# Kernel tuning notes

Measured on AMD Instinct MI355X. Metric: run time of the kernel, lower is better.

## Reference

```python
import jax, jax.numpy as jnp
import numpy as np

H = 2048   # hidden_size
I = 4096   # intermediate_size (expert_dim_per_shard, world_size=1)
E = 8      # num_local_experts


def setup_inputs() -> dict:
    key = jax.random.key(0)
    ks = jax.random.split(key, 7)
    s = 0.02
    return {
        "hidden_states": jax.random.normal(ks[0], (1, 2048, H), dtype=jnp.float32),
        "router_w": jax.random.normal(ks[1], (H, E), dtype=jnp.float32) * s,
        "gate_up_proj": jax.random.normal(ks[2], (E, H, 2 * I), dtype=jnp.float32) * s,
        "down_proj": jax.random.normal(ks[3], (E, I, H), dtype=jnp.float32) * s,
        "shared_gate_w": jax.random.normal(ks[4], (H, I), dtype=jnp.float32) * s,
        "shared_up_w": jax.random.normal(ks[5], (H, I), dtype=jnp.float32) * s,
        "shared_down_w": jax.random.normal(ks[6], (I, H), dtype=jnp.float32) * s,
        "top_k": 1,
    }


def reference(hidden_states, router_w, gate_up_proj, down_proj,
              shared_gate_w, shared_up_w, shared_down_w, top_k):
    b, s, h = hidden_states.shape
    hs = hidden_states.reshape(-1, h)                      # [T, H]
    T = hs.shape[0]

    # router + topk scatter (non-topk -> -inf so sigmoid -> 0)
    logits = hs @ router_w                                 # [T, E]
    top_v, top_i = jax.lax.top_k(logits, top_k)            # [T, k]
    neg_inf = jnp.full_like(logits, -jnp.inf)
    rows = jnp.arange(T)[:, None]
    router_scores = neg_inf.at[rows, top_i].set(top_v).T   # [E, T]
    router_scores = jax.nn.sigmoid(router_scores.astype(jnp.float32)).astype(hs.dtype)

    # dense dispatch: every token to every expert, scaled by (mostly zero) scores
    routed_in = hs[None, :, :] * router_scores[:, :, None]  # [E, T, H]

    # per-expert grouped GEMM (SwiGLU)
    gate_up = jnp.einsum('eth,ehf->etf', routed_in, gate_up_proj)  # [E, T, 2I]
    gate, up = jnp.split(gate_up, 2, axis=-1)
    routed_out = jnp.einsum('eti,eih->eth', up * jax.nn.silu(gate), down_proj)  # [E, T, H]

    # shared expert (SwiGLU MLP)
    shared = (jax.nn.silu(hs @ shared_gate_w) * (hs @ shared_up_w)) @ shared_down_w  # [T, H]

    # scatter_add over arange indices == sum over experts
    out = shared + routed_out.sum(axis=0)                  # [T, H]
    return out, router_scores
```

## Files before the change

### kernel.cpp

```cpp
#include <hip/hip_runtime.h>
#include <hip/hip_bf16.h>

#define H_DIM 2048
#define E_NUM 8
#define I_DIM 4096
#define TWO_I 8192
#define T_TOK 2048

#define BM 256
#define BN 64
#define BK 64

typedef __bf16 bf16x8 __attribute__((ext_vector_type(8)));
typedef float f32x4 __attribute__((ext_vector_type(4)));

static __device__ __forceinline__ unsigned short f2bs(float x) {
    __hip_bfloat16 h = __float2bfloat16(x);
    return __builtin_bit_cast(unsigned short, h);
}

#define GLL(gsrc, ldst) __builtin_amdgcn_global_load_lds( \
    (const __attribute__((address_space(1))) void*)(gsrc), \
    (__attribute__((address_space(3))) void*)(ldst), 16, 0, 0)

#define MFMA16(a, b, c) __builtin_amdgcn_mfma_f32_16x16x32_bf16(a, b, c, 0, 0, 0)
#define BSWZ(n) (((((n) & 7) ^ (((n) >> 2) & 7))) << 4)
#define A_SRC_CHUNK(lane) ((((lane) & 7) ^ (((lane) >> 3) & 7)) * 8)
#define BARRIER() asm volatile("s_waitcnt lgkmcnt(0)\ns_barrier" ::: "memory")

static __device__ __forceinline__ bf16x8 bload(
    const unsigned short* __restrict__ Bs, int n, int s, int h) {
    int off = (n * 128 + s * 64 + h * 16) ^ BSWZ(n);
    return *reinterpret_cast<const bf16x8*>((const char*)Bs + off);
}

static __device__ __forceinline__ bf16x8 aload(
    const unsigned short* __restrict__ As, int row, int s, int h) {
    int off = row * 128 + ((s * 64 + h * 16) ^ ((row & 7) << 4));
    return *reinterpret_cast<const bf16x8*>((const char*)As + off);
}

__global__ __launch_bounds__(256) void router_convert_kernel(
    const float* __restrict__ hs, const float* __restrict__ rw,
    float* __restrict__ out_scores, int* __restrict__ eidx,
    unsigned short* __restrict__ xb, unsigned short* __restrict__ xs) {
    int tok = blockIdx.x * 4 + (threadIdx.x >> 6);
    int lane = threadIdx.x & 63;
    const float* row = hs + (size_t)tok * H_DIM;
    float4 v[8];
    float acc[E_NUM];
#pragma unroll
    for (int e = 0; e < E_NUM; e++) acc[e] = 0.f;
#pragma unroll
    for (int i = 0; i < 8; i++) {
        int hb = i * 256 + lane * 4;
        v[i] = *reinterpret_cast<const float4*>(row + hb);
        const float* w0 = rw + (size_t)hb * E_NUM;
#pragma unroll
        for (int e = 0; e < E_NUM; e++) {
            acc[e] += v[i].x * w0[e] + v[i].y * w0[E_NUM + e] +
                      v[i].z * w0[2 * E_NUM + e] + v[i].w * w0[3 * E_NUM + e];
        }
    }
#pragma unroll
    for (int e = 0; e < E_NUM; e++) {
#pragma unroll
        for (int o = 32; o > 0; o >>= 1) acc[e] += __shfl_xor(acc[e], o, 64);
    }
    int best = 0; float bv = acc[0];
#pragma unroll
    for (int e = 1; e < E_NUM; e++) { if (acc[e] > bv) { bv = acc[e]; best = e; } }
    float sc = 1.f / (1.f + expf(-bv));
    if (lane < E_NUM) out_scores[(size_t)lane * T_TOK + tok] = (lane == best) ? sc : 0.f;
    if (lane == 0) eidx[tok] = best;
    unsigned short* xbr = xb + (size_t)tok * H_DIM;
    unsigned short* xsr = xs + (size_t)tok * H_DIM;
#pragma unroll
    for (int i = 0; i < 8; i++) {
        int hb = i * 256 + lane * 4;
        ushort4 b, s4;
        b.x = f2bs(v[i].x); b.y = f2bs(v[i].y); b.z = f2bs(v[i].z); b.w = f2bs(v[i].w);
        s4.x = f2bs(v[i].x * sc); s4.y = f2bs(v[i].y * sc);
        s4.z = f2bs(v[i].z * sc); s4.w = f2bs(v[i].w * sc);
        *reinterpret_cast<ushort4*>(xbr + hb) = b;
        *reinterpret_cast<ushort4*>(xsr + hb) = s4;
    }
}

__global__ void group_kernel(const int* __restrict__ eidx, int* __restrict__ perm,
                             int* __restrict__ off) {
    __shared__ int cnt[E_NUM];
    __shared__ int base[E_NUM];
    int t = threadIdx.x;
    if (t < E_NUM) cnt[t] = 0;
    __syncthreads();
    for (int i = t; i < T_TOK; i += 256) atomicAdd(&cnt[eidx[i]], 1);
    __syncthreads();
    if (t == 0) {
        int s = 0;
        for (int e = 0; e < E_NUM; e++) { base[e] = s; off[e] = s; s += cnt[e]; }
        off[E_NUM] = s;
    }
    __syncthreads();
    for (int i = t; i < T_TOK; i += 256) {
        int e = eidx[i];
        int p = atomicAdd(&base[e], 1);
        perm[p] = i;
    }
}

__global__ __launch_bounds__(256, 2) void gemm1_kernel(
    const unsigned short* __restrict__ xb, const unsigned short* __restrict__ xs,
    const float* __restrict__ gup, const float* __restrict__ sg,
    const float* __restrict__ su, const int* __restrict__ perm,
    const int* __restrict__ off, unsigned short* __restrict__ hmid) {
    int nt = blockIdx.x;
    int g = blockIdx.y >> 3;
    int mt = blockIdx.y & 7;
    int rowbase, ng;
    if (g < E_NUM) { rowbase = off[g]; ng = off[g + 1] - rowbase; }
    else { rowbase = 0; ng = T_TOK; }
    int mstart = mt * BM;
    if (mstart >= ng) return;

    __shared__ unsigned short As[2][BM * BK];
    __shared__ unsigned short Bg[BN * BK];
    __shared__ unsigned short Bu[BN * BK];

    int tid = threadIdx.x;
    int wave = tid >> 6, lane = tid & 63;
    int h = lane >> 4, ln = lane & 15;

    const unsigned short* Abase = (g == E_NUM) ? xb : xs;
    unsigned int aoff[8];
#pragma unroll
    for (int j = 0; j < 8; j++) {
        int r = wave * 64 + j * 8 + (lane >> 3);
        int sr = mstart + r; sr = (sr < ng) ? sr : (ng - 1);
        int tokr = (g < E_NUM) ? perm[rowbase + sr] : sr;
        aoff[j] = (unsigned int)tokr * H_DIM + A_SRC_CHUNK(lane);
    }
    int n0 = nt * BN;
    const float* gbase;
    const float* ubase;
    size_t ldb;
    if (g < E_NUM) {
        gbase = gup + (size_t)g * H_DIM * TWO_I + n0;
        ubase = gbase + I_DIM;
        ldb = TWO_I;
    } else {
        gbase = sg + n0;
        ubase = su + n0;
        ldb = I_DIM;
    }
    int k0i = wave * 16 + ((lane >> 4) << 2);
    int nb = (lane & 15) << 2;
    const float* pg = gbase + (size_t)k0i * ldb + nb;
    const float* pu = ubase + (size_t)k0i * ldb + nb;

    f32x4 zero = {0.f, 0.f, 0.f, 0.f};
    f32x4 accg[4][4], accu[4][4];
#pragma unroll
    for (int i = 0; i < 4; i++)
#pragma unroll
        for (int j = 0; j < 4; j++) { accg[i][j] = zero; accu[i][j] = zero; }

    const int NT = H_DIM / BK;
    f32x4 qg0, qg1, qg2, qg3, qu0, qu1, qu2, qu3;

#define G1_QLOAD(t_) { size_t ko_ = (size_t)(t_) * BK * ldb; \
        const float* p_ = pg + ko_; \
        qg0 = *reinterpret_cast<const f32x4*>(p_); \
        qg1 = *reinterpret_cast<const f32x4*>(p_ + ldb); \
        qg2 = *reinterpret_cast<const f32x4*>(p_ + 2 * ldb); \
        qg3 = *reinterpret_cast<const f32x4*>(p_ + 3 * ldb); \
        p_ = pu + ko_; \
        qu0 = *reinterpret_cast<const f32x4*>(p_); \
        qu1 = *reinterpret_cast<const f32x4*>(p_ + ldb); \
        qu2 = *reinterpret_cast<const f32x4*>(p_ + 2 * ldb); \
        qu3 = *reinterpret_cast<const f32x4*>(p_ + 3 * ldb); }
#define G1_BWRITE() { _Pragma("unroll") \
        for (int i_ = 0; i_ < 4; i_++) { int n_ = nb + i_; \
            ushort4 og_, ou_; \
            og_.x = f2bs(qg0[i_]); og_.y = f2bs(qg1[i_]); \
            og_.z = f2bs(qg2[i_]); og_.w = f2bs(qg3[i_]); \
            ou_.x = f2bs(qu0[i_]); ou_.y = f2bs(qu1[i_]); \
            ou_.z = f2bs(qu2[i_]); ou_.w = f2bs(qu3[i_]); \
            int ob_ = (n_ * 128 + k0i * 2) ^ BSWZ(n_); \
            *reinterpret_cast<ushort4*>((char*)Bg + ob_) = og_; \
            *reinterpret_cast<ushort4*>((char*)Bu + ob_) = ou_; } }
#define G1_AGLL(t_, buf_) { _Pragma("unroll") \
        for (int j_ = 0; j_ < 8; j_++) \
            GLL(Abase + aoff[j_] + (unsigned)(t_) * BK, \
                &As[buf_][(wave * 64 + j_ * 8) * BK]); }

    G1_QLOAD(0);
    G1_AGLL(0, 0);
    asm volatile("s_waitcnt vmcnt(0)" ::: "memory");
    G1_BWRITE();
    G1_AGLL(1, 1);
    G1_QLOAD(1);
    BARRIER();

    for (int t = 0; t < NT; ++t) {
        const unsigned short* Ab = &As[t & 1][0];
#pragma unroll
        for (int s = 0; s < 2; s++) {
            bf16x8 a0 = aload(Ab, wave * 64 + 0 * 16 + ln, s, h);
            bf16x8 a1 = aload(Ab, wave * 64 + 1 * 16 + ln, s, h);
            bf16x8 a2 = aload(Ab, wave * 64 + 2 * 16 + ln, s, h);
            bf16x8 a3 = aload(Ab, wave * 64 + 3 * 16 + ln, s, h);
#pragma unroll
            for (int j = 0; j < 4; j++) {
                bf16x8 bg = bload(Bg, j * 16 + ln, s, h);
                accg[0][j] = MFMA16(a0, bg, accg[0][j]);
                accg[1][j] = MFMA16(a1, bg, accg[1][j]);
                accg[2][j] = MFMA16(a2, bg, accg[2][j]);
                accg[3][j] = MFMA16(a3, bg, accg[3][j]);
            }
#pragma unroll
            for (int j = 0; j < 4; j++) {
                bf16x8 bu = bload(Bu, j * 16 + ln, s, h);
                accu[0][j] = MFMA16(a0, bu, accu[0][j]);
                accu[1][j] = MFMA16(a1, bu, accu[1][j]);
                accu[2][j] = MFMA16(a2, bu, accu[2][j]);
                accu[3][j] = MFMA16(a3, bu, accu[3][j]);
            }
        }
        BARRIER();
        if (t + 1 < NT) {
            G1_BWRITE();
            int tc = t + 2; if (tc > NT - 1) tc = NT - 1;
            G1_AGLL(tc, t & 1);
            G1_QLOAD(tc);
            BARRIER();
        }
    }

    int hbase = (g < E_NUM) ? rowbase : T_TOK;
#pragma unroll
    for (int i = 0; i < 4; i++) {
#pragma unroll
        for (int j = 0; j < 4; j++) {
#pragma unroll
            for (int r = 0; r < 4; r++) {
                int row = wave * 64 + i * 16 + h * 4 + r;
                int sr = mstart + row;
                if (sr < ng) {
                    float gv = accg[i][j][r], uv = accu[i][j][r];
                    float hv = gv / (1.f + expf(-gv)) * uv;
                    int col = n0 + j * 16 + ln;
                    hmid[(size_t)(hbase + sr) * I_DIM + col] = f2bs(hv);
                }
            }
        }
    }
}

template <int ADD>
__global__ __launch_bounds__(256, 2) void gemm2_kernel(
    const unsigned short* __restrict__ hmid, const float* __restrict__ dwn,
    const float* __restrict__ sd, const int* __restrict__ perm,
    const int* __restrict__ off, float* __restrict__ out) {
    int nt = blockIdx.x;
    int g, mt, rowbase, ng, hbase;
    if (ADD) {
        g = blockIdx.y >> 3; mt = blockIdx.y & 7;
        rowbase = off[g]; ng = off[g + 1] - rowbase; hbase = rowbase;
    } else {
        g = E_NUM; mt = blockIdx.y; rowbase = 0; ng = T_TOK; hbase = T_TOK;
    }
    int mstart = mt * BM;
    if (mstart >= ng) return;

    __shared__ unsigned short As[2][BM * BK];
    __shared__ unsigned short Bs[BN * BK];

    int tid = threadIdx.x;
    int wave = tid >> 6, lane = tid & 63;
    int h = lane >> 4, ln = lane & 15;

    unsigned int aoff[8];
#pragma unroll
    for (int j = 0; j < 8; j++) {
        int r = wave * 64 + j * 8 + (lane >> 3);
        int sr = mstart + r; sr = (sr < ng) ? sr : (ng - 1);
        aoff[j] = (unsigned int)(hbase + sr) * I_DIM + A_SRC_CHUNK(lane);
    }
    int n0 = nt * BN;
    const float* bbase = ADD ? (dwn + (size_t)g * I_DIM * H_DIM + n0) : (sd + n0);
    const size_t ldb = H_DIM;
    int k0i = wave * 16 + ((lane >> 4) << 2);
    int nb = (lane & 15) << 2;
    const float* pb = bbase + (size_t)k0i * ldb + nb;

    f32x4 zero = {0.f, 0.f, 0.f, 0.f};
    f32x4 acc[4][4];
#pragma unroll
    for (int i = 0; i < 4; i++)
#pragma unroll
        for (int j = 0; j < 4; j++) acc[i][j] = zero;

    const int NT2 = I_DIM / BK;
    f32x4 qb0, qb1, qb2, qb3;

#define G2_QLOAD(t_) { size_t ko_ = (size_t)(t_) * BK * ldb; \
        const float* p_ = pb + ko_; \
        qb0 = *reinterpret_cast<const f32x4*>(p_); \
        qb1 = *reinterpret_cast<const f32x4*>(p_ + ldb); \
        qb2 = *reinterpret_cast<const f32x4*>(p_ + 2 * ldb); \
        qb3 = *reinterpret_cast<const f32x4*>(p_ + 3 * ldb); }
#define G2_BWRITE() { _Pragma("unroll") \
        for (int i_ = 0; i_ < 4; i_++) { int n_ = nb + i_; \
            ushort4 o_; \
            o_.x = f2bs(qb0[i_]); o_.y = f2bs(qb1[i_]); \
            o_.z = f2bs(qb2[i_]); o_.w = f2bs(qb3[i_]); \
            int ob_ = (n_ * 128 + k0i * 2) ^ BSWZ(n_); \
            *reinterpret_cast<ushort4*>((char*)Bs + ob_) = o_; } }
#define G2_AGLL(t_, buf_) { _Pragma("unroll") \
        for (int j_ = 0; j_ < 8; j_++) \
            GLL(hmid + aoff[j_] + (unsigned)(t_) * BK, \
                &As[buf_][(wave * 64 + j_ * 8) * BK]); }

    G2_QLOAD(0);
    G2_AGLL(0, 0);
    asm volatile("s_waitcnt vmcnt(0)" ::: "memory");
    G2_BWRITE();
    G2_AGLL(1, 1);
    G2_QLOAD(1);
    BARRIER();

    for (int t = 0; t < NT2; ++t) {
        const unsigned short* Ab = &As[t & 1][0];
#pragma unroll
        for (int s = 0; s < 2; s++) {
            bf16x8 a0 = aload(Ab, wave * 64 + 0 * 16 + ln, s, h);
            bf16x8 a1 = aload(Ab, wave * 64 + 1 * 16 + ln, s, h);
            bf16x8 a2 = aload(Ab, wave * 64 + 2 * 16 + ln, s, h);
            bf16x8 a3 = aload(Ab, wave * 64 + 3 * 16 + ln, s, h);
#pragma unroll
            for (int j = 0; j < 4; j++) {
                bf16x8 b = bload(Bs, j * 16 + ln, s, h);
                acc[0][j] = MFMA16(a0, b, acc[0][j]);
                acc[1][j] = MFMA16(a1, b, acc[1][j]);
                acc[2][j] = MFMA16(a2, b, acc[2][j]);
                acc[3][j] = MFMA16(a3, b, acc[3][j]);
            }
        }
        BARRIER();
        if (t + 1 < NT2) {
            G2_BWRITE();
            int tc = t + 2; if (tc > NT2 - 1) tc = NT2 - 1;
            G2_AGLL(tc, t & 1);
            G2_QLOAD(tc);
            BARRIER();
        }
    }

#pragma unroll
    for (int i = 0; i < 4; i++) {
#pragma unroll
        for (int j = 0; j < 4; j++) {
#pragma unroll
            for (int r = 0; r < 4; r++) {
                int row = wave * 64 + i * 16 + h * 4 + r;
                int sr = mstart + row;
                if (sr < ng) {
                    int tok = ADD ? perm[rowbase + sr] : sr;
                    int col = n0 + j * 16 + ln;
                    float v = acc[i][j][r];
                    float* o = out + (size_t)tok * H_DIM + col;
                    if (ADD) *o += v; else *o = v;
                }
            }
        }
    }
}

extern "C" void kernel_launch(void* const* d_in, const int* in_sizes, int n_in,
                              void* d_out, int out_size, void* d_ws, size_t ws_size,
                              hipStream_t stream) {
    (void)in_sizes; (void)n_in; (void)out_size;
    const float* hs  = (const float*)d_in[0];
    const float* rw  = (const float*)d_in[1];
    const float* gup = (const float*)d_in[2];
    const float* dwn = (const float*)d_in[3];
    const float* sg  = (const float*)d_in[4];
    const float* su  = (const float*)d_in[5];
    const float* sd  = (const float*)d_in[6];
    float* out = (float*)d_out;
    float* out_scores = out + (size_t)T_TOK * H_DIM;

    char* w = (char*)d_ws;
    size_t o = 0;
    auto alloc = [&](size_t bytes) {
        void* p = w + o;
        o += (bytes + 255) & ~(size_t)255;
        return p;
    };
    unsigned short* xb   = (unsigned short*)alloc((size_t)T_TOK * H_DIM * 2);
    unsigned short* xs   = (unsigned short*)alloc((size_t)T_TOK * H_DIM * 2);
    unsigned short* hmid = (unsigned short*)alloc((size_t)2 * T_TOK * I_DIM * 2);
    int* eidx    = (int*)alloc(T_TOK * 4);
    int* perm    = (int*)alloc(T_TOK * 4);
    int* off     = (int*)alloc(64 * 4);
    if (ws_size < o) return;

    router_convert_kernel<<<T_TOK / 4, 256, 0, stream>>>(hs, rw, out_scores, eidx, xb, xs);
    group_kernel<<<1, 256, 0, stream>>>(eidx, perm, off);

    gemm1_kernel<<<dim3(I_DIM / BN, 9 * 8), 256, 0, stream>>>(
        xb, xs, gup, sg, su, perm, off, hmid);
    gemm2_kernel<0><<<dim3(H_DIM / BN, 8), 256, 0, stream>>>(hmid, dwn, sd, perm, off, out);
    gemm2_kernel<1><<<dim3(H_DIM / BN, E_NUM * 8), 256, 0, stream>>>(hmid, dwn, sd, perm, off, out);
}
```

Before: 507.9 us.

## Deepen B-weight register prefetch to two stages with partial vmcnt waits

Both GEMM kernels now keep two register sets of fp32 weight tiles in flight, prefetching the B tile three K-steps ahead instead of two. The main loop is unrolled by two so the register sets alternate, and explicit s_waitcnt vmcnt(N) waits allow only the oldest loads to complete before compute. The aim is to hide global load latency for the fp32 weight stream, which dominates memory traffic. This costs extra VGPRs, which may hurt occupancy at launch bounds of 2 blocks. The hand-counted vmcnt values must match the actual number of outstanding loads.

```diff
diff --git a/kernel.cpp b/kernel.cpp
--- a/kernel.cpp
+++ b/kernel.cpp
@@ -27,6 +27,7 @@
 #define BSWZ(n) (((((n) & 7) ^ (((n) >> 2) & 7))) << 4)
 #define A_SRC_CHUNK(lane) ((((lane) & 7) ^ (((lane) >> 3) & 7)) * 8)
 #define BARRIER() asm volatile("s_waitcnt lgkmcnt(0)\ns_barrier" ::: "memory")
+#define FENCE() asm volatile("" ::: "memory")
 
 static __device__ __forceinline__ bf16x8 bload(
     const unsigned short* __restrict__ Bs, int n, int s, int h) {
@@ -124,8 +125,8 @@
     if (mstart >= ng) return;
 
     __shared__ unsigned short As[2][BM * BK];
-    __shared__ unsigned short Bg[BN * BK];
-    __shared__ unsigned short Bu[BN * BK];
+    __shared__ unsigned short LBg[BN * BK];
+    __shared__ unsigned short LBu[BN * BK];
 
     int tid = threadIdx.x;
     int wave = tid >> 6, lane = tid & 63;
@@ -166,75 +167,85 @@
         for (int j = 0; j < 4; j++) { accg[i][j] = zero; accu[i][j] = zero; }
 
     const int NT = H_DIM / BK;
-    f32x4 qg0, qg1, qg2, qg3, qu0, qu1, qu2, qu3;
-
-#define G1_QLOAD(t_) { size_t ko_ = (size_t)(t_) * BK * ldb; \
+    f32x4 qag0, qag1, qag2, qag3, qau0, qau1, qau2, qau3;
+    f32x4 qbg0, qbg1, qbg2, qbg3, qbu0, qbu1, qbu2, qbu3;
+
+#define G1_QLOAD(t_, G0,G1,G2,G3, U0,U1,U2,U3) { \
+        size_t ko_ = (size_t)(t_) * BK * ldb; \
         const float* p_ = pg + ko_; \
-        qg0 = *reinterpret_cast<const f32x4*>(p_); \
-        qg1 = *reinterpret_cast<const f32x4*>(p_ + ldb); \
-        qg2 = *reinterpret_cast<const f32x4*>(p_ + 2 * ldb); \
-        qg3 = *reinterpret_cast<const f32x4*>(p_ + 3 * ldb); \
+        G0 = *reinterpret_cast<const f32x4*>(p_); \
+        G1 = *reinterpret_cast<const f32x4*>(p_ + ldb); \
+        G2 = *reinterpret_cast<const f32x4*>(p_ + 2 * ldb); \
+        G3 = *reinterpret_cast<const f32x4*>(p_ + 3 * ldb); \
         p_ = pu + ko_; \
-        qu0 = *reinterpret_cast<const f32x4*>(p_); \
-        qu1 = *reinterpret_cast<const f32x4*>(p_ + ldb); \
-        qu2 = *reinterpret_cast<const f32x4*>(p_ + 2 * ldb); \
-        qu3 = *reinterpret_cast<const f32x4*>(p_ + 3 * ldb); }
-#define G1_BWRITE() { _Pragma("unroll") \
+        U0 = *reinterpret_cast<const f32x4*>(p_); \
+        U1 = *reinterpret_cast<const f32x4*>(p_ + ldb); \
+        U2 = *reinterpret_cast<const f32x4*>(p_ + 2 * ldb); \
+        U3 = *reinterpret_cast<const f32x4*>(p_ + 3 * ldb); }
+#define G1_BWRITE(G0,G1,G2,G3, U0,U1,U2,U3) { _Pragma("unroll") \
         for (int i_ = 0; i_ < 4; i_++) { int n_ = nb + i_; \
             ushort4 og_, ou_; \
-            og_.x = f2bs(qg0[i_]); og_.y = f2bs(qg1[i_]); \
-            og_.z = f2bs(qg2[i_]); og_.w = f2bs(qg3[i_]); \
-            ou_.x = f2bs(qu0[i_]); ou_.y = f2bs(qu1[i_]); \
-            ou_.z = f2bs(qu2[i_]); ou_.w = f2bs(qu3[i_]); \
+            og_.x = f2bs(G0[i_]); og_.y = f2bs(G1[i_]); \
+            og_.z = f2bs(G2[i_]); og_.w = f2bs(G3[i_]); \
+            ou_.x = f2bs(U0[i_]); ou_.y = f2bs(U1[i_]); \
+            ou_.z = f2bs(U2[i_]); ou_.w = f2bs(U3[i_]); \
             int ob_ = (n_ * 128 + k0i * 2) ^ BSWZ(n_); \
-            *reinterpret_cast<ushort4*>((char*)Bg + ob_) = og_; \
-            *reinterpret_cast<ushort4*>((char*)Bu + ob_) = ou_; } }
+            *reinterpret_cast<ushort4*>((char*)LBg + ob_) = og_; \
+            *reinterpret_cast<ushort4*>((char*)LBu + ob_) = ou_; } }
 #define G1_AGLL(t_, buf_) { _Pragma("unroll") \
         for (int j_ = 0; j_ < 8; j_++) \
             GLL(Abase + aoff[j_] + (unsigned)(t_) * BK, \
                 &As[buf_][(wave * 64 + j_ * 8) * BK]); }
-
-    G1_QLOAD(0);
+#define G1_COMPUTE(buf_) { const unsigned short* Ab_ = &As[buf_][0]; \
+        _Pragma("unroll") \
+        for (int s_ = 0; s_ < 2; s_++) { \
+            bf16x8 a0_ = aload(Ab_, wave * 64 + 0 * 16 + ln, s_, h); \
+            bf16x8 a1_ = aload(Ab_, wave * 64 + 1 * 16 + ln, s_, h); \
+            bf16x8 a2_ = aload(Ab_, wave * 64 + 2 * 16 + ln, s_, h); \
+            bf16x8 a3_ = aload(Ab_, wave * 64 + 3 * 16 + ln, s_, h); \
+            _Pragma("unroll") \
+            for (int j_ = 0; j_ < 4; j_++) { \
+                bf16x8 wg_ = bload(LBg, j_ * 16 + ln, s_, h); \
+                accg[0][j_] = MFMA16(a0_, wg_, accg[0][j_]); \
+                accg[1][j_] = MFMA16(a1_, wg_, accg[1][j_]); \
+                accg[2][j_] = MFMA16(a2_, wg_, accg[2][j_]); \
+                accg[3][j_] = MFMA16(a3_, wg_, accg[3][j_]); \
+            } \
+            _Pragma("unroll") \
+            for (int j_ = 0; j_ < 4; j_++) { \
+                bf16x8 wu_ = bload(LBu, j_ * 16 + ln, s_, h); \
+                accu[0][j_] = MFMA16(a0_, wu_, accu[0][j_]); \
+                accu[1][j_] = MFMA16(a1_, wu_, accu[1][j_]); \
+                accu[2][j_] = MFMA16(a2_, wu_, accu[2][j_]); \
+                accu[3][j_] = MFMA16(a3_, wu_, accu[3][j_]); \
+            } \
+        } }
+#define G1_SEG(t_, buf_, G0,G1,G2,G3, U0,U1,U2,U3) { \
+        asm volatile("s_waitcnt vmcnt(20)" ::: "memory"); \
+        G1_COMPUTE(buf_); \
+        BARRIER(); \
+        G1_BWRITE(G0,G1,G2,G3, U0,U1,U2,U3); \
+        FENCE(); \
+        { int tc_ = (t_) + 2; if (tc_ > NT - 1) tc_ = NT - 1; G1_AGLL(tc_, buf_); } \
+        FENCE(); \
+        { int tq_ = (t_) + 3; if (tq_ > NT - 1) tq_ = NT - 1; \
+          G1_QLOAD(tq_, G0,G1,G2,G3, U0,U1,U2,U3); } \
+        BARRIER(); }
+
+    G1_QLOAD(0, qag0,qag1,qag2,qag3, qau0,qau1,qau2,qau3);
     G1_AGLL(0, 0);
-    asm volatile("s_waitcnt vmcnt(0)" ::: "memory");
-    G1_BWRITE();
+    FENCE();
+    G1_BWRITE(qag0,qag1,qag2,qag3, qau0,qau1,qau2,qau3);
+    FENCE();
     G1_AGLL(1, 1);
-    G1_QLOAD(1);
+    FENCE();
+    G1_QLOAD(1, qag0,qag1,qag2,qag3, qau0,qau1,qau2,qau3);
+    G1_QLOAD(2, qbg0,qbg1,qbg2,qbg3, qbu0,qbu1,qbu2,qbu3);
     BARRIER();
 
-    for (int t = 0; t < NT; ++t) {
-        const unsigned short* Ab = &As[t & 1][0];
-#pragma unroll
-        for (int s = 0; s < 2; s++) {
-            bf16x8 a0 = aload(Ab, wave * 64 + 0 * 16 + ln, s, h);
-            bf16x8 a1 = aload(Ab, wave * 64 + 1 * 16 + ln, s, h);
-            bf16x8 a2 = aload(Ab, wave * 64 + 2 * 16 + ln, s, h);
-            bf16x8 a3 = aload(Ab, wave * 64 + 3 * 16 + ln, s, h);
-#pragma unroll
-            for (int j = 0; j < 4; j++) {
-                bf16x8 bg = bload(Bg, j * 16 + ln, s, h);
-                accg[0][j] = MFMA16(a0, bg, accg[0][j]);
-                accg[1][j] = MFMA16(a1, bg, accg[1][j]);
-                accg[2][j] = MFMA16(a2, bg, accg[2][j]);
-                accg[3][j] = MFMA16(a3, bg, accg[3][j]);
-            }
-#pragma unroll
-            for (int j = 0; j < 4; j++) {
-                bf16x8 bu = bload(Bu, j * 16 + ln, s, h);
-                accu[0][j] = MFMA16(a0, bu, accu[0][j]);
-                accu[1][j] = MFMA16(a1, bu, accu[1][j]);
-                accu[2][j] = MFMA16(a2, bu, accu[2][j]);
-                accu[3][j] = MFMA16(a3, bu, accu[3][j]);
-            }
-        }
-        BARRIER();
-        if (t + 1 < NT) {
-            G1_BWRITE();
-            int tc = t + 2; if (tc > NT - 1) tc = NT - 1;
-            G1_AGLL(tc, t & 1);
-            G1_QLOAD(tc);
-            BARRIER();
-        }
+    for (int t = 0; t < NT; t += 2) {
+        G1_SEG(t,     0, qag0,qag1,qag2,qag3, qau0,qau1,qau2,qau3)
+        G1_SEG(t + 1, 1, qbg0,qbg1,qbg2,qbg3, qbu0,qbu1,qbu2,qbu3)
     }
 
     int hbase = (g < E_NUM) ? rowbase : T_TOK;
@@ -274,7 +285,7 @@
     if (mstart >= ng) return;
 
     __shared__ unsigned short As[2][BM * BK];
-    __shared__ unsigned short Bs[BN * BK];
+    __shared__ unsigned short LBs[BN * BK];
 
     int tid = threadIdx.x;
     int wave = tid >> 6, lane = tid & 63;
@@ -302,59 +313,67 @@
         for (int j = 0; j < 4; j++) acc[i][j] = zero;
 
     const int NT2 = I_DIM / BK;
-    f32x4 qb0, qb1, qb2, qb3;
-
-#define G2_QLOAD(t_) { size_t ko_ = (size_t)(t_) * BK * ldb; \
+    f32x4 qa0, qa1, qa2, qa3, qb0, qb1, qb2, qb3;
+
+#define G2_QLOAD(t_, Q0,Q1,Q2,Q3) { size_t ko_ = (size_t)(t_) * BK * ldb; \
         const float* p_ = pb + ko_; \
-        qb0 = *reinterpret_cast<const f32x4*>(p_); \
-        qb1 = *reinterpret_cast<const f32x4*>(p_ + ldb); \
-        qb2 = *reinterpret_cast<const f32x4*>(p_ + 2 * ldb); \
-        qb3 = *reinterpret_cast<const f32x4*>(p_ + 3 * ldb); }
-#define G2_BWRITE() { _Pragma("unroll") \
+        Q0 = *reinterpret_cast<const f32x4*>(p_); \
+        Q1 = *reinterpret_cast<const f32x4*>(p_ + ldb); \
+        Q2 = *reinterpret_cast<const f32x4*>(p_ + 2 * ldb); \
+        Q3 = *reinterpret_cast<const f32x4*>(p_ + 3 * ldb); }
+#define G2_BWRITE(Q0,Q1,Q2,Q3) { _Pragma("unroll") \
         for (int i_ = 0; i_ < 4; i_++) { int n_ = nb + i_; \
             ushort4 o_; \
-            o_.x = f2bs(qb0[i_]); o_.y = f2bs(qb1[i_]); \
-            o_.z = f2bs(qb2[i_]); o_.w = f2bs(qb3[i_]); \
+            o_.x = f2bs(Q0[i_]); o_.y = f2bs(Q1[i_]); \
+            o_.z = f2bs(Q2[i_]); o_.w = f2bs(Q3[i_]); \
             int ob_ = (n_ * 128 + k0i * 2) ^ BSWZ(n_); \
-            *reinterpret_cast<ushort4*>((char*)Bs + ob_) = o_; } }
+            *reinterpret_cast<ushort4*>((char*)LBs + ob_) = o_; } }
 #define G2_AGLL(t_, buf_) { _Pragma("unroll") \
         for (int j_ = 0; j_ < 8; j_++) \
             GLL(hmid + aoff[j_] + (unsigned)(t_) * BK, \
                 &As[buf_][(wave * 64 + j_ * 8) * BK]); }
-
-    G2_QLOAD(0);
+#define G2_COMPUTE(buf_) { const unsigned short* Ab_ = &As[buf_][0]; \
+        _Pragma("unroll") \
+        for (int s_ = 0; s_ < 2; s_++) { \
+            bf16x8 a0_ = aload(Ab_, wave * 64 + 0 * 16 + ln, s_, h); \
+            bf16x8 a1_ = aload(Ab_, wave * 64 + 1 * 16 + ln, s_, h); \
+            bf16x8 a2_ = aload(Ab_, wave * 64 + 2 * 16 + ln, s_, h); \
+            bf16x8 a3_ = aload(Ab_, wave * 64 + 3 * 16 + ln, s_, h); \
+            _Pragma("unroll") \
+            for (int j_ = 0; j_ < 4; j_++) { \
+                bf16x8 wb_ = bload(LBs, j_ * 16 + ln, s_, h); \
+                acc[0][j_] = MFMA16(a0_, wb_, acc[0][j_]); \
+                acc[1][j_] = MFMA16(a1_, wb_, acc[1][j_]); \
+                acc[2][j_] = MFMA16(a2_, wb_, acc[2][j_]); \
+                acc[3][j_] = MFMA16(a3_, wb_, acc[3][j_]); \
+            } \
+        } }
+#define G2_SEG(t_, buf_, Q0,Q1,Q2,Q3) { \
+        asm volatile("s_waitcnt vmcnt(16)" ::: "memory"); \
+        G2_COMPUTE(buf_); \
+        BARRIER(); \
+        G2_BWRITE(Q0,Q1,Q2,Q3); \
+        FENCE(); \
+        { int tc_ = (t_) + 2; if (tc_ > NT2 - 1) tc_ = NT2 - 1; G2_AGLL(tc_, buf_); } \
+        FENCE(); \
+        { int tq_ = (t_) + 3; if (tq_ > NT2 - 1) tq_ = NT2 - 1; \
+          G2_QLOAD(tq_, Q0,Q1,Q2,Q3); } \
+        BARRIER(); }
+
+    G2_QLOAD(0, qa0,qa1,qa2,qa3);
     G2_AGLL(0, 0);
-    asm volatile("s_waitcnt vmcnt(0)" ::: "memory");
-    G2_BWRITE();
+    FENCE();
+    G2_BWRITE(qa0,qa1,qa2,qa3);
+    FENCE();
     G2_AGLL(1, 1);
-    G2_QLOAD(1);
+    FENCE();
+    G2_QLOAD(1, qa0,qa1,qa2,qa3);
+    G2_QLOAD(2, qb0,qb1,qb2,qb3);
     BARRIER();
 
-    for (int t = 0; t < NT2; ++t) {
-        const unsigned short* Ab = &As[t & 1][0];
-#pragma unroll
-        for (int s = 0; s < 2; s++) {
-            bf16x8 a0 = aload(Ab, wave * 64 + 0 * 16 + ln, s, h);
-            bf16x8 a1 = aload(Ab, wave * 64 + 1 * 16 + ln, s, h);
-            bf16x8 a2 = aload(Ab, wave * 64 + 2 * 16 + ln, s, h);
-            bf16x8 a3 = aload(Ab, wave * 64 + 3 * 16 + ln, s, h);
-#pragma unroll
-            for (int j = 0; j < 4; j++) {
-                bf16x8 b = bload(Bs, j * 16 + ln, s, h);
-                acc[0][j] = MFMA16(a0, b, acc[0][j]);
-                acc[1][j] = MFMA16(a1, b, acc[1][j]);
-                acc[2][j] = MFMA16(a2, b, acc[2][j]);
-                acc[3][j] = MFMA16(a3, b, acc[3][j]);
-            }
-        }
-        BARRIER();
-        if (t + 1 < NT2) {
-            G2_BWRITE();
-            int tc = t + 2; if (tc > NT2 - 1) tc = NT2 - 1;
-            G2_AGLL(tc, t & 1);
-            G2_QLOAD(tc);
-            BARRIER();
-        }
+    for (int t = 0; t < NT2; t += 2) {
+        G2_SEG(t,     0, qa0,qa1,qa2,qa3)
+        G2_SEG(t + 1, 1, qb0,qb1,qb2,qb3)
     }
 
 #pragma unroll
```

Result: slower. 997.7 us (+96.4%).
